# Kernel tuning notes

Hardware: AMD Instinct MI355X
Metric: run time of the kernel (lower is better)

Reference implementation:

```python
import math
import jax, jax.numpy as jnp
import numpy as np

NUM_HEAD = 16

def get_slopes(n):
    def pow2(n):
        start = 2 ** (-2 ** (-(math.log2(n) - 3)))
        return [start * start ** i for i in range(n)]
    if math.log2(n).is_integer():
        return pow2(n)
    c = 2 ** math.floor(math.log2(n))
    return pow2(c) + get_slopes(2 * c)[0::2][: n - c]

def setup_inputs() -> dict:
    key = jax.random.key(0)
    ks = jax.random.split(key, 9)
    B, T, C = 2, 2048, 2048
    x = jax.random.normal(ks[0], (B, T, C), dtype=jnp.float32)
    std = 0.02
    Wq = std * jax.random.normal(ks[1], (C, C), dtype=jnp.float32)
    Wk = std * jax.random.normal(ks[2], (C, C), dtype=jnp.float32)
    Wv = std * jax.random.normal(ks[3], (C, C), dtype=jnp.float32)
    Wo = (0.02 / np.sqrt(2 * 24)) * jax.random.normal(ks[4], (C, C), dtype=jnp.float32)
    bq = jnp.zeros((C,), jnp.float32)
    bk = jnp.zeros((C,), jnp.float32)
    bv = jnp.zeros((C,), jnp.float32)
    bo = jnp.zeros((C,), jnp.float32)
    return {"x": x, "Wq": Wq, "bq": bq, "Wk": Wk, "bk": bk,
            "Wv": Wv, "bv": bv, "Wo": Wo, "bo": bo}

def reference(x, Wq, bq, Wk, bk, Wv, bv, Wo, bo):
    B, T, C = x.shape
    H = NUM_HEAD
    D = C // H
    slopes = jnp.asarray(get_slopes(H), dtype=jnp.float32)  # [H]

    def split_heads(y):  # [B,T,C] -> [B,H,T,D]
        return y.reshape(B, T, H, D).transpose(0, 2, 1, 3)

    q = split_heads(x @ Wq + bq)
    k = split_heads(x @ Wk + bk)
    v = split_heads(x @ Wv + bv)

    attn = jnp.einsum("bhqd,bhkd->bhqk", q, k) / jnp.sqrt(jnp.float32(D))
    # ALiBi: bias[h, j] = slopes[h] * (j - (T-1)), broadcast over queries
    alibi = slopes[:, None, None] * (jnp.arange(T, dtype=jnp.float32) - (T - 1))[None, None, :]
    attn = attn + alibi  # [B,H,T,T] + [H,1,T]

    causal = jnp.tril(jnp.ones((T, T), dtype=bool))[None, None]
    attn = jnp.where(causal, attn, jnp.finfo(jnp.float32).min)
    p = jax.nn.softmax(attn, axis=-1)

    o = jnp.einsum("bhqk,bhkd->bhqd", p, v).transpose(0, 2, 1, 3).reshape(B, T, C)
    return o @ Wo + bo
```

## Files before the change

kernel.cpp:

```cpp
#include <hip/hip_runtime.h>
#include <math.h>


typedef unsigned short u16;
using bf16x8 = __attribute__((ext_vector_type(8))) short;
using f32x4  = __attribute__((ext_vector_type(4))) float;

__device__ __forceinline__ u16 f2bf(float f) {
  union { float f; unsigned u; } c; c.f = f;
  unsigned r = c.u + 0x7fffu + ((c.u >> 16) & 1u);
  return (u16)(r >> 16);
}
__device__ __forceinline__ float bf2f(u16 b) {
  union { unsigned u; float f; } c; c.u = ((unsigned)b) << 16; return c.f;
}
__device__ __forceinline__ unsigned cvtpk(float a, float b) {
  unsigned r;
  asm("v_cvt_pk_bf16_f32 %0, %1, %2" : "=v"(r) : "v"(a), "v"(b));
  return r;
}
__device__ __forceinline__ void g2l16(const void* g, void* l) {
  __builtin_amdgcn_global_load_lds(
      (const __attribute__((address_space(1))) void*)g,
      (__attribute__((address_space(3))) void*)l, 16, 0, 0);
}

__device__ __forceinline__ int band_jmin(int s, float slope2) {
  const int idist = (int)(36.0f / slope2);
  const int cut = 64 * s - idist - 31;
  return (cut > 0) ? (cut >> 5) : 0;
}

__global__ __launch_bounds__(256) void split_f32(const float* __restrict__ in,
                                                 u16* __restrict__ hi, int n4) {
  for (int i = blockIdx.x * 256 + threadIdx.x; i < n4; i += gridDim.x * 256) {
    const float4 v = ((const float4*)in)[i];
    ushort4 h;
    h.x = f2bf(v.x); h.y = f2bf(v.y); h.z = f2bf(v.z); h.w = f2bf(v.w);
    ((ushort4*)hi)[i] = h;
  }
}

__global__ __launch_bounds__(256) void tsplit4_f32(
    const float* __restrict__ W0, const float* __restrict__ W1,
    const float* __restrict__ W2, const float* __restrict__ W3,
    u16* __restrict__ D0, u16* __restrict__ D1,
    u16* __restrict__ D2, u16* __restrict__ D3,
    int N, int K, float sc0) {
  __shared__ float tile[64][68];
  const int z = blockIdx.z;
  const float* W = (z == 0) ? W0 : (z == 1) ? W1 : (z == 2) ? W2 : W3;
  u16* Wth = (z == 0) ? D0 : (z == 1) ? D1 : (z == 2) ? D2 : D3;
  const float sc = (z == 0) ? sc0 : 1.f;
  const int tid = threadIdx.x;
  const int k0 = blockIdx.y * 64, n0 = blockIdx.x * 64;
  const int rr = tid >> 4, cc = (tid & 15) * 4;
#pragma unroll
  for (int u = 0; u < 4; ++u) {
    const float4 v = *(const float4*)&W[(size_t)(k0 + rr + 16 * u) * N + n0 + cc];
    tile[rr + 16 * u][cc + 0] = v.x;
    tile[rr + 16 * u][cc + 1] = v.y;
    tile[rr + 16 * u][cc + 2] = v.z;
    tile[rr + 16 * u][cc + 3] = v.w;
  }
  __syncthreads();
#pragma unroll
  for (int u = 0; u < 4; ++u) {
    const int nn = rr + 16 * u;
    ushort4 h;
    h.x = f2bf(tile[cc + 0][nn] * sc);
    h.y = f2bf(tile[cc + 1][nn] * sc);
    h.z = f2bf(tile[cc + 2][nn] * sc);
    h.w = f2bf(tile[cc + 3][nn] * sc);
    *(ushort4*)&Wth[(size_t)(n0 + nn) * K + k0 + cc] = h;
  }
}

template <int MODE>
__global__ __launch_bounds__(512, 2) void gemm256(
    const u16* __restrict__ Ah, const u16* __restrict__ Bth,
    const float* __restrict__ bias, const float* __restrict__ bias2,
    float bsc, u16* __restrict__ outH, u16* __restrict__ outH2,
    float* __restrict__ outF, int MM, int NN, int KK) {
  __shared__ u16 LA[2][2][8192];
  __shared__ u16 LB[2][2][8192];

  const int tid = threadIdx.x;
  const int wave = tid >> 6, lane = tid & 63;
  const int g = lane >> 4, q15 = lane & 15;
  const int wr = wave >> 2, wc = wave & 3;
  const int m0 = blockIdx.y * 256, n0 = blockIdx.x * 256;
  const int NT = KK >> 6;

  f32x4 acc[8][4];
#pragma unroll
  for (int f = 0; f < 8; ++f)
#pragma unroll
    for (int j = 0; j < 4; ++j) acc[f][j] = (f32x4){0.f, 0.f, 0.f, 0.f};

  auto stageA = [&](int t, int hh) {
#pragma unroll
    for (int l = 0; l < 2; ++l) {
      const int ch = l * 512 + tid;
      const int row = ch >> 3, slot = ch & 7;
      const size_t ga = (size_t)(m0 + hh * 128 + row) * KK + t * 64 +
                        ((slot ^ (row & 7)) * 8);
      g2l16(Ah + ga, (char*)(LA[t & 1][hh]) + ch * 16);
    }
  };
  auto stageB = [&](int t, int hh) {
#pragma unroll
    for (int l = 0; l < 2; ++l) {
      const int ch = l * 512 + tid;
      const int row = ch >> 3, slot = ch & 7;
      const size_t gb = (size_t)(n0 + hh * 128 + row) * KK + t * 64 +
                        ((slot ^ (row & 7)) * 8);
      g2l16(Bth + gb, (char*)(LB[t & 1][hh]) + ch * 16);
    }
  };

  stageA(0, 0); stageA(0, 1); stageB(0, 0); stageB(0, 1);
  asm volatile("s_waitcnt vmcnt(0)" ::: "memory");
  __builtin_amdgcn_sched_barrier(0);
  __builtin_amdgcn_s_barrier();

  for (int t = 0; t < NT; ++t) {
    const int d = t & 1;
    const char* baseA = (const char*)(LA[d][wr]);
    const char* baseB = (const char*)(LB[d][wc >> 1]);
    const int rbBase = (wc & 1) * 64;
    const int sx = q15 & 7;
#pragma unroll
    for (int p = 0; p < 4; ++p) {
      const int mh = p >> 1, nh = p & 1;
      bf16x8 af[4][2], bf[2][2];
#pragma unroll
      for (int f = 0; f < 4; ++f) {
        const int rowh = mh * 64 + f * 16 + q15;
#pragma unroll
        for (int kk = 0; kk < 2; ++kk)
          af[f][kk] = *(const bf16x8*)(baseA + rowh * 128 +
                                       (((kk * 4 + g) ^ sx) * 16));
      }
#pragma unroll
      for (int j = 0; j < 2; ++j) {
        const int rowh = rbBase + nh * 32 + j * 16 + q15;
#pragma unroll
        for (int kk = 0; kk < 2; ++kk)
          bf[j][kk] = *(const bf16x8*)(baseB + rowh * 128 +
                                       (((kk * 4 + g) ^ sx) * 16));
      }
      if (t + 1 < NT) {
        if (p == 0) { stageA(t + 1, 0); stageA(t + 1, 1); }
        else if (p == 1) stageB(t + 1, 0);
        else if (p == 2) stageB(t + 1, 1);
      }
      __builtin_amdgcn_sched_barrier(0);
      __builtin_amdgcn_s_barrier();
      asm volatile("s_waitcnt lgkmcnt(0)" ::: "memory");
      __builtin_amdgcn_sched_barrier(0);
      __builtin_amdgcn_s_setprio(1);
#pragma unroll
      for (int f = 0; f < 4; ++f)
#pragma unroll
        for (int j = 0; j < 2; ++j)
#pragma unroll
          for (int kk = 0; kk < 2; ++kk)
            acc[mh * 4 + f][nh * 2 + j] = __builtin_amdgcn_mfma_f32_16x16x32_bf16(
                af[f][kk], bf[j][kk], acc[mh * 4 + f][nh * 2 + j], 0, 0, 0);
      __builtin_amdgcn_s_setprio(0);
      if (p == 3) {
        asm volatile("s_waitcnt vmcnt(0)" ::: "memory");
      }
      __builtin_amdgcn_sched_barrier(0);
      __builtin_amdgcn_s_barrier();
    }
  }

#pragma unroll
  for (int f = 0; f < 8; ++f)
#pragma unroll
    for (int j = 0; j < 4; ++j)
#pragma unroll
      for (int r = 0; r < 4; ++r) {
        const int row = m0 + wr * 128 + f * 16 + g * 4 + r;
        const int col = n0 + wc * 64 + j * 16 + q15;
        const float v = acc[f][j][r];
        if (MODE == 3) {
          const int sel = col >> 11;
          const int c2 = col & 2047;
          const float vv = v + (sel ? bias2[c2] : bias[c2] * bsc);
          const int bb = row >> 11, tt = row & 2047;
          const int hh = c2 >> 7, dd = c2 & 127;
          (sel ? outH2 : outH)[(((size_t)bb * 16 + hh) * 2048 + tt) * 128 + dd] =
              f2bf(vv);
        }
      }
}

template <int MODE>
__global__ __launch_bounds__(512) void gemm256x128(
    const u16* __restrict__ Ah, const u16* __restrict__ Bth,
    const float* __restrict__ bias, float bsc,
    u16* __restrict__ outH, float* __restrict__ outF,
    int MM, int NN, int KK) {
  __shared__ u16 LA[2][2][8192];
  __shared__ u16 LB[2][8192];

  const int tid = threadIdx.x;
  const int wave = tid >> 6, lane = tid & 63;
  const int g = lane >> 4, q15 = lane & 15;
  const int wr = wave >> 1, wc = wave & 1;
  const int m0 = blockIdx.y * 256, n0 = blockIdx.x * 128;
  const int NT = KK >> 6;

  f32x4 acc[4][4];
#pragma unroll
  for (int f = 0; f < 4; ++f)
#pragma unroll
    for (int j = 0; j < 4; ++j) acc[f][j] = (f32x4){0.f, 0.f, 0.f, 0.f};

  auto stageA = [&](int t, int hh) {
#pragma unroll
    for (int l = 0; l < 2; ++l) {
      const int ch = l * 512 + tid;
      const int row = ch >> 3, slot = ch & 7;
      const size_t ga = (size_t)(m0 + hh * 128 + row) * KK + t * 64 +
                        ((slot ^ (row & 7)) * 8);
      g2l16(Ah + ga, (char*)(LA[t & 1][hh]) + ch * 16);
    }
  };
  auto stageB = [&](int t) {
#pragma unroll
    for (int l = 0; l < 2; ++l) {
      const int ch = l * 512 + tid;
      const int row = ch >> 3, slot = ch & 7;
      const size_t gb = (size_t)(n0 + row) * KK + t * 64 +
                        ((slot ^ (row & 7)) * 8);
      g2l16(Bth + gb, (char*)(LB[t & 1]) + ch * 16);
    }
  };

  stageA(0, 0); stageA(0, 1); stageB(0);
  asm volatile("s_waitcnt vmcnt(0)" ::: "memory");
  __builtin_amdgcn_sched_barrier(0);
  __builtin_amdgcn_s_barrier();

  for (int t = 0; t < NT; ++t) {
    const int d = t & 1;
    const char* baseA = (const char*)(LA[d][wr >> 1]);
    const int raBase = (wr & 1) * 64;
    const char* baseB = (const char*)(LB[d]);
    const int rbBase = wc * 64;
    const int sx = q15 & 7;
#pragma unroll
    for (int p = 0; p < 4; ++p) {
      const int mq = p >> 1, nq = p & 1;
      bf16x8 af[2][2], bf[2][2];
#pragma unroll
      for (int f = 0; f < 2; ++f) {
        const int rowh = raBase + mq * 32 + f * 16 + q15;
#pragma unroll
        for (int kk = 0; kk < 2; ++kk)
          af[f][kk] = *(const bf16x8*)(baseA + rowh * 128 +
                                       (((kk * 4 + g) ^ sx) * 16));
      }
#pragma unroll
      for (int j = 0; j < 2; ++j) {
        const int rowh = rbBase + nq * 32 + j * 16 + q15;
#pragma unroll
        for (int kk = 0; kk < 2; ++kk)
          bf[j][kk] = *(const bf16x8*)(baseB + rowh * 128 +
                                       (((kk * 4 + g) ^ sx) * 16));
      }
      if (t + 1 < NT) {
        if (p == 0) stageA(t + 1, 0);
        else if (p == 1) stageA(t + 1, 1);
        else if (p == 2) stageB(t + 1);
      }
      __builtin_amdgcn_sched_barrier(0);
      __builtin_amdgcn_s_barrier();
      asm volatile("s_waitcnt lgkmcnt(0)" ::: "memory");
      __builtin_amdgcn_sched_barrier(0);
      __builtin_amdgcn_s_setprio(1);
#pragma unroll
      for (int f = 0; f < 2; ++f)
#pragma unroll
        for (int j = 0; j < 2; ++j)
#pragma unroll
          for (int kk = 0; kk < 2; ++kk)
            acc[mq * 2 + f][nq * 2 + j] = __builtin_amdgcn_mfma_f32_16x16x32_bf16(
                af[f][kk], bf[j][kk], acc[mq * 2 + f][nq * 2 + j], 0, 0, 0);
      __builtin_amdgcn_s_setprio(0);
      if (p == 3) {
        asm volatile("s_waitcnt vmcnt(0)" ::: "memory");
      }
      __builtin_amdgcn_sched_barrier(0);
      __builtin_amdgcn_s_barrier();
    }
  }

#pragma unroll
  for (int f = 0; f < 4; ++f)
#pragma unroll
    for (int j = 0; j < 4; ++j)
#pragma unroll
      for (int r = 0; r < 4; ++r) {
        const int row = m0 + wr * 64 + f * 16 + g * 4 + r;
        const int col = n0 + wc * 64 + j * 16 + q15;
        const float v = acc[f][j][r];
        if (MODE == 0) {
          outF[(size_t)row * NN + col] = v + bias[col] * bsc;
        } else {
          outH[(size_t)row * NN + col] = f2bf(v + bias[row] * bsc);
        }
      }
}

__global__ __launch_bounds__(128) void attn_splitk(
    const u16* __restrict__ Qh, const u16* __restrict__ Kh,
    const u16* __restrict__ Vth, u16* __restrict__ Oh,
    float* __restrict__ Obuf, float* __restrict__ mArr,
    float* __restrict__ lArr, int T, int NB, int BH) {
  __shared__ u16 KS[3][4096];

  const int tid = threadIdx.x;
  const int wid = tid >> 6, lane = tid & 63;
  const int g = lane >> 4, q15 = lane & 15;
  const int L = blockIdx.x;

  int bh, u;
  if (BH == 32) {
    const int k = L >> 8;
    const int c = L & 255;
    bh = (c + 5 * k) & 31;
    u = k * 8 + (c >> 5);
  } else {
    bh = L / 48;
    u = L % 48;
  }
  int s, half;
  if (u < 16)      { s = u;      half = 2; }
  else if (u < 32) { s = 47 - u; half = 0; }
  else             { s = 63 - u; half = 1; }

  const int b = bh >> 4, h = bh & 15;
  const float slope2 = exp2f(-0.5f * (float)(h + 1)) * 1.44269504f;
  const int jmin = band_jmin(s, slope2);
  const bool loEmpty = (jmin >= s + 1);

  if (half == 0 && loEmpty) return;

  int lo, hi;
  if (half == 2)      { lo = jmin;                hi = 2 * s + 2; }
  else if (half == 0) { lo = jmin;                hi = s + 1; }
  else                { lo = loEmpty ? jmin : (s + 1); hi = 2 * s + 2; }
  const int ns = hi - lo;
  const bool maskable = (half != 0);
  const bool normStore = (half == 2) || (half == 1 && loEmpty);

  const int qw0 = s * 64 + wid * 32;
  const size_t vrow0 = (size_t)h * 128;
  const size_t vcol0 = (size_t)b * T;
  const size_t kbase = (size_t)bh * T;

  bf16x8 qfr[2][4];
#pragma unroll
  for (int qf2 = 0; qf2 < 2; ++qf2) {
    const size_t rb = ((size_t)bh * T + qw0 + qf2 * 16 + q15) * 128;
#pragma unroll
    for (int ks = 0; ks < 4; ++ks)
      qfr[qf2][ks] = *(const bf16x8*)&Qh[rb + ks * 32 + g * 8];
  }

  f32x4 oacc[2][8];
#pragma unroll
  for (int a = 0; a < 2; ++a)
#pragma unroll
    for (int n = 0; n < 8; ++n) oacc[a][n] = (f32x4){0.f, 0.f, 0.f, 0.f};
  float m_st[2] = {-1e5f, -1e5f};
  float l_part[2] = {0.f, 0.f};

  float sc8[2][4];
#pragma unroll
  for (int jf = 0; jf < 2; ++jf)
#pragma unroll
    for (int r = 0; r < 4; ++r) sc8[jf][r] = slope2 * (float)(jf * 16 + r);

  auto stageK = [&](int jt, int bf) {
    const int j0 = jt * 32;
#pragma unroll
    for (int uu = 0; uu < 4; ++uu) {
      const int c = wid * 4 + uu;
      const int row = c * 4 + g;
      const int off = (q15 * 16) ^ ((row & 7) << 4);
      const size_t gb = (kbase + j0 + row) * 128;
      g2l16((const char*)(Kh + gb) + off, (char*)(KS[bf]) + c * 1024);
    }
  };
  auto loadV = [&](int jt, bf16x8 (&vf)[8]) {
    const int j0 = jt * 32;
#pragma unroll
    for (int nf = 0; nf < 8; ++nf)
      vf[nf] = *(const bf16x8*)
          &Vth[(vrow0 + nf * 16 + q15) * (size_t)NB + vcol0 + j0 + g * 8];
  };

  bf16x8 vfA[8], vfB[8];
  __builtin_amdgcn_sched_barrier(0);
  stageK(hi - 1, 0);
  if (ns > 1) stageK(hi - 2, 1);
  __builtin_amdgcn_sched_barrier(0);
  loadV(hi - 1, vfA);
  asm volatile("s_waitcnt vmcnt(8)" ::: "memory");
  __builtin_amdgcn_sched_barrier(0);

  int cur = 0;

  auto ITER = [&](int it, bf16x8 (&vc)[8], bf16x8 (&vn)[8]) {
    const int jt = hi - 1 - it;
    const int j0 = jt * 32;
    __builtin_amdgcn_s_barrier();
    __builtin_amdgcn_sched_barrier(0);

    const bool haveV1 = (it + 1 < ns);
    const bool haveK2 = (it + 2 < ns);
    if (haveV1) loadV(jt - 1, vn);
    if (haveK2) {
      int nb = cur + 2; if (nb >= 3) nb -= 3;
      stageK(jt - 2, nb);
    }
    __builtin_amdgcn_sched_barrier(0);

    f32x4 sacc[2][2];
#pragma unroll
    for (int jf = 0; jf < 2; ++jf)
#pragma unroll
      for (int qf2 = 0; qf2 < 2; ++qf2) sacc[jf][qf2] = (f32x4){0.f, 0.f, 0.f, 0.f};
#pragma unroll
    for (int ks = 0; ks < 4; ++ks) {
      bf16x8 ka[2];
#pragma unroll
      for (int jf = 0; jf < 2; ++jf) {
        const int row = jf * 16 + q15;
        const int off = (row * 256 + ks * 64 + g * 16) ^ ((row & 7) << 4);
        ka[jf] = *(const bf16x8*)((const char*)(KS[cur]) + off);
      }
#pragma unroll
      for (int jf = 0; jf < 2; ++jf)
#pragma unroll
        for (int qf2 = 0; qf2 < 2; ++qf2)
          sacc[jf][qf2] = __builtin_amdgcn_mfma_f32_16x16x32_bf16(
              ka[jf], qfr[qf2][ks], sacc[jf][qf2], 0, 0, 0);
    }

    float a8[2][4];
    const float jb = (float)(j0 + 4 * g - (T - 1));
#pragma unroll
    for (int jf = 0; jf < 2; ++jf)
#pragma unroll
      for (int r = 0; r < 4; ++r) a8[jf][r] = fmaf(slope2, jb, sc8[jf][r]);

    unsigned Fw[2][4];
#pragma unroll
    for (int qf2 = 0; qf2 < 2; ++qf2) {
      const int qg = qw0 + qf2 * 16 + q15;
      float sv[2][4];
      float mt = -1e30f;
#pragma unroll
      for (int jf = 0; jf < 2; ++jf)
#pragma unroll
        for (int r = 0; r < 4; ++r) {
          float x = sacc[jf][qf2][r] + a8[jf][r];
          if (maskable && it < 2) {
            const int jg = j0 + jf * 16 + 4 * g + r;
            x = (jg > qg) ? -1e30f : x;
          }
          sv[jf][r] = x;
          mt = fmaxf(mt, x);
        }
      if (!__all(mt <= m_st[qf2] + 11.0f)) {
        mt = fmaxf(mt, __shfl_xor(mt, 16));
        mt = fmaxf(mt, __shfl_xor(mt, 32));
        const float mnew = fmaxf(m_st[qf2], mt);
        const float scl = exp2f(m_st[qf2] - mnew);
        l_part[qf2] *= scl;
        m_st[qf2] = mnew;
#pragma unroll
        for (int r = 0; r < 4; ++r) {
          const float sc = __shfl(scl, g * 4 + r);
#pragma unroll
          for (int nf = 0; nf < 8; ++nf) oacc[qf2][nf][r] *= sc;
        }
      }
      float rs = 0.f;
      float p[2][4];
#pragma unroll
      for (int jf = 0; jf < 2; ++jf)
#pragma unroll
        for (int r = 0; r < 4; ++r) {
          p[jf][r] = exp2f(sv[jf][r] - m_st[qf2]);
          rs += p[jf][r];
        }
      l_part[qf2] += rs;
      const unsigned W00 = cvtpk(p[0][0], p[0][1]), W01 = cvtpk(p[0][2], p[0][3]);
      const unsigned W10 = cvtpk(p[1][0], p[1][1]), W11 = cvtpk(p[1][2], p[1][3]);
      const int srcA = q15 + ((g & 1) << 5);
      const int srcB = srcA + 16;
      const unsigned A0 = (unsigned)__shfl((int)W00, srcA);
      const unsigned A1 = (unsigned)__shfl((int)W01, srcA);
      const unsigned B0 = (unsigned)__shfl((int)W00, srcB);
      const unsigned B1 = (unsigned)__shfl((int)W01, srcB);
      const unsigned C0 = (unsigned)__shfl((int)W10, srcA);
      const unsigned C1 = (unsigned)__shfl((int)W11, srcA);
      const unsigned D0 = (unsigned)__shfl((int)W10, srcB);
      const unsigned D1 = (unsigned)__shfl((int)W11, srcB);
      const bool hi2 = g >= 2;
      Fw[qf2][0] = hi2 ? C0 : A0;
      Fw[qf2][1] = hi2 ? C1 : A1;
      Fw[qf2][2] = hi2 ? D0 : B0;
      Fw[qf2][3] = hi2 ? D1 : B1;
    }

    if (haveV1) {
      if (haveK2) { asm volatile("s_waitcnt vmcnt(12)" ::: "memory"); }
      else        { asm volatile("s_waitcnt vmcnt(8)"  ::: "memory"); }
    } else        { asm volatile("s_waitcnt vmcnt(0)"  ::: "memory"); }
    __builtin_amdgcn_sched_barrier(0);

    union { unsigned uu[4]; bf16x8 v; } pa0, pa1;
#pragma unroll
    for (int w = 0; w < 4; ++w) { pa0.uu[w] = Fw[0][w]; pa1.uu[w] = Fw[1][w]; }
#pragma unroll
    for (int nf = 0; nf < 8; ++nf) {
      oacc[0][nf] = __builtin_amdgcn_mfma_f32_16x16x32_bf16(pa0.v, vc[nf], oacc[0][nf], 0, 0, 0);
      oacc[1][nf] = __builtin_amdgcn_mfma_f32_16x16x32_bf16(pa1.v, vc[nf], oacc[1][nf], 0, 0, 0);
    }

    cur = (cur == 2) ? 0 : cur + 1;
  };

  for (int it = 0; it < ns;) {
    ITER(it, vfA, vfB); ++it;
    if (it >= ns) break;
    ITER(it, vfB, vfA); ++it;
  }

  float lrow[2];
#pragma unroll
  for (int qf2 = 0; qf2 < 2; ++qf2) {
    float lr = l_part[qf2];
    lr += __shfl_xor(lr, 16);
    lr += __shfl_xor(lr, 32);
    lrow[qf2] = lr;
  }

  if (normStore) {
#pragma unroll
    for (int qf2 = 0; qf2 < 2; ++qf2) {
      const float inv = 1.0f / lrow[qf2];
#pragma unroll
      for (int r = 0; r < 4; ++r) {
        const float iv = __shfl(inv, g * 4 + r);
        const int qrow = qw0 + qf2 * 16 + g * 4 + r;
        const size_t ob = ((size_t)b * T + qrow) * 2048 + h * 128;
#pragma unroll
        for (int nf = 0; nf < 8; ++nf)
          Oh[ob + nf * 16 + q15] = f2bf(oacc[qf2][nf][r] * iv);
      }
    }
  } else {
    const int sp = s - 16;
    const size_t sbase = ((size_t)(bh * 16 + sp) * 2 + half) * 64;
    if (g == 0) {
#pragma unroll
      for (int qf2 = 0; qf2 < 2; ++qf2) {
        mArr[sbase + wid * 32 + qf2 * 16 + q15] = m_st[qf2];
        lArr[sbase + wid * 32 + qf2 * 16 + q15] = lrow[qf2];
      }
    }
    const size_t obase = sbase * 128;
#pragma unroll
    for (int qf2 = 0; qf2 < 2; ++qf2)
#pragma unroll
      for (int r = 0; r < 4; ++r) {
        const int row = wid * 32 + qf2 * 16 + g * 4 + r;
#pragma unroll
        for (int nf = 0; nf < 8; ++nf)
          Obuf[obase + (size_t)row * 128 + nf * 16 + q15] = oacc[qf2][nf][r];
      }
  }
}

__global__ __launch_bounds__(128) void combine_halves(
    const float* __restrict__ Obuf, const float* __restrict__ mArr,
    const float* __restrict__ lArr, u16* __restrict__ Oh, int T) {
  const int idx = blockIdx.x;
  const int row = idx & 63;
  const int sp = (idx >> 6) & 15;
  const int bh = idx >> 10;
  const int d = threadIdx.x;
  const int s = sp + 16;
  const int b = bh >> 4, h = bh & 15;
  const float slope2 = exp2f(-0.5f * (float)(h + 1)) * 1.44269504f;
  if (band_jmin(s, slope2) >= s + 1) return;
  const size_t sbase = ((size_t)(bh * 16 + sp) * 2) * 64;
  const float m1 = mArr[sbase + row],      l1 = lArr[sbase + row];
  const float m2 = mArr[sbase + 64 + row], l2 = lArr[sbase + 64 + row];
  const float M = fmaxf(m1, m2);
  const float w1 = exp2f(m1 - M), w2 = exp2f(m2 - M);
  const float inv = 1.0f / (l1 * w1 + l2 * w2);
  const size_t ob = sbase * 128;
  const float o1 = Obuf[ob + (size_t)row * 128 + d];
  const float o2 = Obuf[ob + 8192 + (size_t)row * 128 + d];
  const float v = (o1 * w1 + o2 * w2) * inv;
  const int qrow = s * 64 + row;
  Oh[((size_t)b * T + qrow) * 2048 + h * 128 + d] = f2bf(v);
}

#define TM 128
#define BKG 8

template <int QKV>
__global__ __launch_bounds__(256) void gemm_f32(
    const float* __restrict__ A, const float* __restrict__ W,
    const float* __restrict__ bias, float* __restrict__ out,
    int M, int N, int K, int T) {
  __shared__ float As[BKG][TM];
  __shared__ float Bs[BKG][TM];
  const int tid = threadIdx.x;
  const int tx = tid & 15, ty = tid >> 4;
  const int m0 = blockIdx.y * TM, n0 = blockIdx.x * TM;
  float acc[8][8];
#pragma unroll
  for (int i = 0; i < 8; ++i)
#pragma unroll
    for (int j = 0; j < 8; ++j) acc[i][j] = 0.f;
  const int arow = tid >> 1, acol = (tid & 1) * 4;
  const int brow = tid >> 5, bcol = (tid & 31) * 4;
  for (int k0 = 0; k0 < K; k0 += BKG) {
    const float4 av = *(const float4*)&A[(size_t)(m0 + arow) * K + k0 + acol];
    const float4 bv = *(const float4*)&W[(size_t)(k0 + brow) * N + n0 + bcol];
    __syncthreads();
    As[acol + 0][arow] = av.x; As[acol + 1][arow] = av.y;
    As[acol + 2][arow] = av.z; As[acol + 3][arow] = av.w;
    *(float4*)&Bs[brow][bcol] = bv;
    __syncthreads();
#pragma unroll
    for (int kk = 0; kk < BKG; ++kk) {
      const float4 a0 = *(const float4*)&As[kk][ty * 4];
      const float4 a1 = *(const float4*)&As[kk][64 + ty * 4];
      const float4 b0 = *(const float4*)&Bs[kk][tx * 4];
      const float4 b1 = *(const float4*)&Bs[kk][64 + tx * 4];
      const float af[8] = {a0.x, a0.y, a0.z, a0.w, a1.x, a1.y, a1.z, a1.w};
      const float bf[8] = {b0.x, b0.y, b0.z, b0.w, b1.x, b1.y, b1.z, b1.w};
#pragma unroll
      for (int i = 0; i < 8; ++i)
#pragma unroll
        for (int j = 0; j < 8; ++j) acc[i][j] += af[i] * bf[j];
    }
  }
#pragma unroll
  for (int a = 0; a < 2; ++a)
#pragma unroll
    for (int i = 0; i < 4; ++i) {
      const int row = m0 + a * 64 + ty * 4 + i;
      const int bb = row / T, t = row % T;
#pragma unroll
      for (int bj = 0; bj < 2; ++bj) {
        const int col = n0 + bj * 64 + tx * 4;
        float4 r;
        r.x = acc[a * 4 + i][bj * 4 + 0] + bias[col + 0];
        r.y = acc[a * 4 + i][bj * 4 + 1] + bias[col + 1];
        r.z = acc[a * 4 + i][bj * 4 + 2] + bias[col + 2];
        r.w = acc[a * 4 + i][bj * 4 + 3] + bias[col + 3];
        if (QKV) {
          const int hh = col >> 7, dd = col & 127;
          *(float4*)&out[(((size_t)bb * 16 + hh) * T + t) * 128 + dd] = r;
        } else {
          *(float4*)&out[(size_t)row * N + col] = r;
        }
      }
    }
}

#define QT 32
#define KT 32
#define DP 132

__global__ __launch_bounds__(256) void flash_f32(
    const float* __restrict__ Q, const float* __restrict__ K,
    const float* __restrict__ V, float* __restrict__ O, int T) {
  __shared__ float Qs[QT][DP];
  __shared__ float Ks[KT][DP];
  __shared__ float Vs[KT][DP];
  __shared__ float Ps[QT][KT + 1];
  const int tid = threadIdx.x;
  const int jh = tid & 15, ih = tid >> 4;
  const int bh = blockIdx.y;
  const int h = bh & 15;
  const int q0 = blockIdx.x * QT;
  const float slope = exp2f(-0.5f * (float)(h + 1));
  const float rsD = 0.08838834764831845f;
  {
    const float* Qg = Q + ((size_t)bh * T + q0) * 128;
    const int r = tid >> 3, p = tid & 7;
#pragma unroll
    for (int u = 0; u < 4; ++u)
      *(float4*)&Qs[r][(p + 8 * u) * 4] = *(const float4*)&Qg[r * 128 + (p + 8 * u) * 4];
  }
  float m_st[2] = {-1e30f, -1e30f};
  float l_st[2] = {0.f, 0.f};
  float accv[2][8] = {};
  const int ktiles = blockIdx.x + 1;
  for (int kt = 0; kt < ktiles; ++kt) {
    const int j0 = kt * KT;
    const float* Kg = K + ((size_t)bh * T + j0) * 128;
    const float* Vg = V + ((size_t)bh * T + j0) * 128;
    __syncthreads();
    {
      const int r = tid >> 3, p = tid & 7;
#pragma unroll
      for (int u = 0; u < 4; ++u) {
        *(float4*)&Ks[r][(p + 8 * u) * 4] = *(const float4*)&Kg[r * 128 + (p + 8 * u) * 4];
        *(float4*)&Vs[r][(p + 8 * u) * 4] = *(const float4*)&Vg[r * 128 + (p + 8 * u) * 4];
      }
    }
    __syncthreads();
    float s00 = 0.f, s01 = 0.f, s10 = 0.f, s11 = 0.f;
#pragma unroll 8
    for (int d4 = 0; d4 < 32; ++d4) {
      const float4 qa = *(const float4*)&Qs[2 * ih + 0][4 * d4];
      const float4 qb = *(const float4*)&Qs[2 * ih + 1][4 * d4];
      const float4 ka = *(const float4*)&Ks[2 * jh + 0][4 * d4];
      const float4 kb = *(const float4*)&Ks[2 * jh + 1][4 * d4];
      s00 += qa.x * ka.x + qa.y * ka.y + qa.z * ka.z + qa.w * ka.w;
      s01 += qa.x * kb.x + qa.y * kb.y + qa.z * kb.z + qa.w * kb.w;
      s10 += qb.x * ka.x + qb.y * ka.y + qb.z * ka.z + qb.w * ka.w;
      s11 += qb.x * kb.x + qb.y * kb.y + qb.z * kb.z + qb.w * kb.w;
    }
    float sc[2][2] = {{s00, s01}, {s10, s11}};
    float mt[2];
#pragma unroll
    for (int r = 0; r < 2; ++r) {
      const int qg = q0 + 2 * ih + r;
#pragma unroll
      for (int c = 0; c < 2; ++c) {
        const int jg = j0 + 2 * jh + c;
        const float svv = sc[r][c] * rsD + slope * (float)(jg - (T - 1));
        sc[r][c] = (jg > qg) ? -1e30f : svv;
      }
      mt[r] = fmaxf(sc[r][0], sc[r][1]);
    }
#pragma unroll
    for (int m = 1; m < 16; m <<= 1) {
      mt[0] = fmaxf(mt[0], __shfl_xor(mt[0], m));
      mt[1] = fmaxf(mt[1], __shfl_xor(mt[1], m));
    }
#pragma unroll
    for (int r = 0; r < 2; ++r) {
      const float mnew = fmaxf(m_st[r], mt[r]);
      const float scl = (m_st[r] > -1e29f) ? expf(m_st[r] - mnew) : 0.f;
      const float p0 = expf(sc[r][0] - mnew);
      const float p1 = expf(sc[r][1] - mnew);
      float rs = p0 + p1;
#pragma unroll
      for (int m = 1; m < 16; m <<= 1) rs += __shfl_xor(rs, m);
      l_st[r] = l_st[r] * scl + rs;
      m_st[r] = mnew;
#pragma unroll
      for (int d = 0; d < 8; ++d) accv[r][d] *= scl;
      Ps[2 * ih + r][2 * jh + 0] = p0;
      Ps[2 * ih + r][2 * jh + 1] = p1;
    }
    __syncthreads();
#pragma unroll 4
    for (int j = 0; j < KT; ++j) {
      const float p0 = Ps[2 * ih + 0][j];
      const float p1 = Ps[2 * ih + 1][j];
      const float4 v0 = *(const float4*)&Vs[j][8 * jh];
      const float4 v1 = *(const float4*)&Vs[j][8 * jh + 4];
      accv[0][0] += p0 * v0.x; accv[0][1] += p0 * v0.y;
      accv[0][2] += p0 * v0.z; accv[0][3] += p0 * v0.w;
      accv[0][4] += p0 * v1.x; accv[0][5] += p0 * v1.y;
      accv[0][6] += p0 * v1.z; accv[0][7] += p0 * v1.w;
      accv[1][0] += p1 * v0.x; accv[1][1] += p1 * v0.y;
      accv[1][2] += p1 * v0.z; accv[1][3] += p1 * v0.w;
      accv[1][4] += p1 * v1.x; accv[1][5] += p1 * v1.y;
      accv[1][6] += p1 * v1.z; accv[1][7] += p1 * v1.w;
    }
  }
  const int b = bh >> 4;
#pragma unroll
  for (int r = 0; r < 2; ++r) {
    const int qg = q0 + 2 * ih + r;
    const float inv = 1.0f / l_st[r];
    float4 o0, o1;
    o0.x = accv[r][0] * inv; o0.y = accv[r][1] * inv;
    o0.z = accv[r][2] * inv; o0.w = accv[r][3] * inv;
    o1.x = accv[r][4] * inv; o1.y = accv[r][5] * inv;
    o1.z = accv[r][6] * inv; o1.w = accv[r][7] * inv;
    float* dst = O + ((size_t)b * T + qg) * 2048 + h * 128 + 8 * jh;
    *(float4*)&dst[0] = o0;
    *(float4*)&dst[4] = o1;
  }
}

extern "C" void kernel_launch(void* const* d_in, const int* in_sizes, int n_in,
                              void* d_out, int out_size, void* d_ws,
                              size_t ws_size, hipStream_t stream) {
  const float* x  = (const float*)d_in[0];
  const float* Wq = (const float*)d_in[1];
  const float* bq = (const float*)d_in[2];
  const float* Wk = (const float*)d_in[3];
  const float* bk = (const float*)d_in[4];
  const float* Wv = (const float*)d_in[5];
  const float* bv = (const float*)d_in[6];
  const float* Wo = (const float*)d_in[7];
  const float* bo = (const float*)d_in[8];
  float* out = (float*)d_out;

  const int C = 2048, T = 2048, H = 16;
  const int M = in_sizes[0] / C;
  const int B = M / T;
  const int BH = B * H;
  const size_t MC = (size_t)M * C, CC = (size_t)C * C;
  const size_t splitO = (size_t)BH * 16 * 2 * 8192;
  const size_t splitML = (size_t)BH * 16 * 2 * 64;
  const size_t need = (5 * MC + 4 * CC) * sizeof(u16) +
                      (splitO + 2 * splitML) * sizeof(float);

  const float QSC = 0.08838834764831845f * 1.44269504088896f;

  if (ws_size >= need && (M % 256) == 0) {
    u16* p = (u16*)d_ws;
    u16* xh   = p; p += MC;
    u16* wqth = p; p += CC;
    u16* wkth = p; p += CC;
    u16* wvth = p; p += CC;
    u16* woth = p; p += CC;
    u16* qh   = p; p += MC;
    u16* kh   = p; p += MC;
    u16* vth  = p; p += MC;
    u16* oh   = p; p += MC;
    float* Obuf = (float*)p;
    float* mArr = Obuf + splitO;
    float* lArr = mArr + splitML;

    split_f32<<<1024, 256, 0, stream>>>(x, xh, (int)(MC / 4));
    dim3 tg(C / 64, C / 64, 4);
    tsplit4_f32<<<tg, 256, 0, stream>>>(Wq, Wk, Wv, Wo, wqth, wkth, wvth,
                                        woth, C, C, QSC);

    dim3 gqk(2 * C / 256, M / 256);
    gemm256<3><<<gqk, 512, 0, stream>>>(xh, wqth, bq, bk, QSC, qh, kh,
                                        nullptr, M, 2 * C, C);
    dim3 gv(M / 128, C / 256);
    gemm256x128<2><<<gv, 512, 0, stream>>>(wvth, xh, bv, 1.f, vth, nullptr,
                                           C, M, C);

    attn_splitk<<<48 * BH, 128, 0, stream>>>(qh, kh, vth, oh, Obuf, mArr,
                                             lArr, T, M, BH);
    combine_halves<<<BH * 16 * 64, 128, 0, stream>>>(Obuf, mArr, lArr, oh, T);

    dim3 gq(C / 128, M / 256);
    gemm256x128<0><<<gq, 512, 0, stream>>>(oh, woth, bo, 1.f, nullptr, out,
                                           M, C, C);
  } else {
    float* Qw = (float*)d_ws;
    float* Kw = Qw + MC;
    float* Vw = Kw + MC;
    float* Ow = Vw + MC;
    dim3 ggrid(C / TM, M / TM);
    gemm_f32<1><<<ggrid, 256, 0, stream>>>(x, Wq, bq, Qw, M, C, C, T);
    gemm_f32<1><<<ggrid, 256, 0, stream>>>(x, Wk, bk, Kw, M, C, C, T);
    gemm_f32<1><<<ggrid, 256, 0, stream>>>(x, Wv, bv, Vw, M, C, C, T);
    dim3 fgrid(T / QT, B * H);
    flash_f32<<<fgrid, 256, 0, stream>>>(Qw, Kw, Vw, Ow, T);
    gemm_f32<0><<<ggrid, 256, 0, stream>>>(Ow, Wo, bo, out, M, C, C, T);
  }
}
```

Before: 315.6 us.

## Use 4-stage LDS ring with K=32 tiles and prefetch depth 3 in GEMMs

Both bf16 GEMM kernels move from a double-buffered K=64 tile to a four-slot ring of K=32 tiles. Global-to-LDS loads are issued three tiles ahead, and partial vmcnt waits replace a full drain every iteration. The LDS swizzle and fragment-load layout change to match the 64-byte rows. This is meant to hide more global memory latency, at the cost of twice as many iterations and barriers, plus more intricate wait-count bookkeeping.

```diff
diff --git a/kernel.cpp b/kernel.cpp
--- a/kernel.cpp
+++ b/kernel.cpp
@@ -82,15 +82,16 @@
     const float* __restrict__ bias, const float* __restrict__ bias2,
     float bsc, u16* __restrict__ outH, u16* __restrict__ outH2,
     float* __restrict__ outF, int MM, int NN, int KK) {
-  __shared__ u16 LA[2][2][8192];
-  __shared__ u16 LB[2][2][8192];
+  __shared__ u16 LA[4][8192];
+  __shared__ u16 LB[4][8192];
 
   const int tid = threadIdx.x;
   const int wave = tid >> 6, lane = tid & 63;
   const int g = lane >> 4, q15 = lane & 15;
   const int wr = wave >> 2, wc = wave & 3;
   const int m0 = blockIdx.y * 256, n0 = blockIdx.x * 256;
-  const int NT = KK >> 6;
+  const int NT = KK >> 5;
+  const int sxg = ((g ^ ((q15 >> 1) & 3)) << 4);
 
   f32x4 acc[8][4];
 #pragma unroll
@@ -98,83 +99,93 @@
 #pragma unroll
     for (int j = 0; j < 4; ++j) acc[f][j] = (f32x4){0.f, 0.f, 0.f, 0.f};
 
-  auto stageA = [&](int t, int hh) {
+  auto stageA = [&](int t) {
+    const int rb = t & 3;
 #pragma unroll
     for (int l = 0; l < 2; ++l) {
       const int ch = l * 512 + tid;
-      const int row = ch >> 3, slot = ch & 7;
-      const size_t ga = (size_t)(m0 + hh * 128 + row) * KK + t * 64 +
-                        ((slot ^ (row & 7)) * 8);
-      g2l16(Ah + ga, (char*)(LA[t & 1][hh]) + ch * 16);
+      const int row = ch >> 2, slot = ch & 3;
+      const size_t ga = (size_t)(m0 + row) * KK + t * 32 +
+                        ((slot ^ ((row >> 1) & 3)) * 8);
+      g2l16(Ah + ga, (char*)(LA[rb]) + ch * 16);
     }
   };
-  auto stageB = [&](int t, int hh) {
+  auto stageB = [&](int t) {
+    const int rb = t & 3;
 #pragma unroll
     for (int l = 0; l < 2; ++l) {
       const int ch = l * 512 + tid;
-      const int row = ch >> 3, slot = ch & 7;
-      const size_t gb = (size_t)(n0 + hh * 128 + row) * KK + t * 64 +
-                        ((slot ^ (row & 7)) * 8);
-      g2l16(Bth + gb, (char*)(LB[t & 1][hh]) + ch * 16);
+      const int row = ch >> 2, slot = ch & 3;
+      const size_t gb = (size_t)(n0 + row) * KK + t * 32 +
+                        ((slot ^ ((row >> 1) & 3)) * 8);
+      g2l16(Bth + gb, (char*)(LB[rb]) + ch * 16);
     }
   };
 
-  stageA(0, 0); stageA(0, 1); stageB(0, 0); stageB(0, 1);
-  asm volatile("s_waitcnt vmcnt(0)" ::: "memory");
+  stageA(0); stageB(0);
+  __builtin_amdgcn_sched_barrier(0);
+  if (NT > 1) { stageA(1); stageB(1); }
+  __builtin_amdgcn_sched_barrier(0);
+  if (NT > 2) { stageA(2); stageB(2); }
+  __builtin_amdgcn_sched_barrier(0);
+  if (NT > 2)      { asm volatile("s_waitcnt vmcnt(8)" ::: "memory"); }
+  else if (NT > 1) { asm volatile("s_waitcnt vmcnt(4)" ::: "memory"); }
+  else             { asm volatile("s_waitcnt vmcnt(0)" ::: "memory"); }
   __builtin_amdgcn_sched_barrier(0);
   __builtin_amdgcn_s_barrier();
 
   for (int t = 0; t < NT; ++t) {
-    const int d = t & 1;
-    const char* baseA = (const char*)(LA[d][wr]);
-    const char* baseB = (const char*)(LB[d][wc >> 1]);
-    const int rbBase = (wc & 1) * 64;
-    const int sx = q15 & 7;
-#pragma unroll
-    for (int p = 0; p < 4; ++p) {
-      const int mh = p >> 1, nh = p & 1;
-      bf16x8 af[4][2], bf[2][2];
-#pragma unroll
-      for (int f = 0; f < 4; ++f) {
-        const int rowh = mh * 64 + f * 16 + q15;
-#pragma unroll
-        for (int kk = 0; kk < 2; ++kk)
-          af[f][kk] = *(const bf16x8*)(baseA + rowh * 128 +
-                                       (((kk * 4 + g) ^ sx) * 16));
-      }
-#pragma unroll
-      for (int j = 0; j < 2; ++j) {
-        const int rowh = rbBase + nh * 32 + j * 16 + q15;
-#pragma unroll
-        for (int kk = 0; kk < 2; ++kk)
-          bf[j][kk] = *(const bf16x8*)(baseB + rowh * 128 +
-                                       (((kk * 4 + g) ^ sx) * 16));
-      }
-      if (t + 1 < NT) {
-        if (p == 0) { stageA(t + 1, 0); stageA(t + 1, 1); }
-        else if (p == 1) stageB(t + 1, 0);
-        else if (p == 2) stageB(t + 1, 1);
-      }
-      __builtin_amdgcn_sched_barrier(0);
-      __builtin_amdgcn_s_barrier();
-      asm volatile("s_waitcnt lgkmcnt(0)" ::: "memory");
-      __builtin_amdgcn_sched_barrier(0);
-      __builtin_amdgcn_s_setprio(1);
-#pragma unroll
-      for (int f = 0; f < 4; ++f)
-#pragma unroll
-        for (int j = 0; j < 2; ++j)
-#pragma unroll
-          for (int kk = 0; kk < 2; ++kk)
-            acc[mh * 4 + f][nh * 2 + j] = __builtin_amdgcn_mfma_f32_16x16x32_bf16(
-                af[f][kk], bf[j][kk], acc[mh * 4 + f][nh * 2 + j], 0, 0, 0);
-      __builtin_amdgcn_s_setprio(0);
-      if (p == 3) {
-        asm volatile("s_waitcnt vmcnt(0)" ::: "memory");
-      }
-      __builtin_amdgcn_sched_barrier(0);
-      __builtin_amdgcn_s_barrier();
-    }
+    const int rb = t & 3;
+    const char* baseA = (const char*)(LA[rb]);
+    const char* baseB = (const char*)(LB[rb]);
+
+    bf16x8 bf[4], af[4];
+#pragma unroll
+    for (int j = 0; j < 4; ++j)
+      bf[j] = *(const bf16x8*)(baseB + (wc * 64 + j * 16 + q15) * 64 + sxg);
+#pragma unroll
+    for (int f = 0; f < 4; ++f)
+      af[f] = *(const bf16x8*)(baseA + (wr * 128 + f * 16 + q15) * 64 + sxg);
+    if (t + 3 < NT) stageA(t + 3);
+    __builtin_amdgcn_sched_barrier(0);
+    __builtin_amdgcn_s_barrier();
+    asm volatile("s_waitcnt lgkmcnt(0)" ::: "memory");
+    __builtin_amdgcn_sched_barrier(0);
+    __builtin_amdgcn_s_setprio(1);
+#pragma unroll
+    for (int f = 0; f < 4; ++f)
+#pragma unroll
+      for (int j = 0; j < 4; ++j)
+        acc[f][j] = __builtin_amdgcn_mfma_f32_16x16x32_bf16(
+            af[f], bf[j], acc[f][j], 0, 0, 0);
+    __builtin_amdgcn_s_setprio(0);
+    __builtin_amdgcn_sched_barrier(0);
+    __builtin_amdgcn_s_barrier();
+
+    bf16x8 ag[4];
+#pragma unroll
+    for (int f = 0; f < 4; ++f)
+      ag[f] = *(const bf16x8*)(baseA + (wr * 128 + 64 + f * 16 + q15) * 64 + sxg);
+    if (t + 3 < NT) stageB(t + 3);
+    __builtin_amdgcn_sched_barrier(0);
+    __builtin_amdgcn_s_barrier();
+    asm volatile("s_waitcnt lgkmcnt(0)" ::: "memory");
+    __builtin_amdgcn_sched_barrier(0);
+    __builtin_amdgcn_s_setprio(1);
+#pragma unroll
+    for (int f = 0; f < 4; ++f)
+#pragma unroll
+      for (int j = 0; j < 4; ++j)
+        acc[4 + f][j] = __builtin_amdgcn_mfma_f32_16x16x32_bf16(
+            ag[f], bf[j], acc[4 + f][j], 0, 0, 0);
+    __builtin_amdgcn_s_setprio(0);
+    if (t + 1 < NT) {
+      if (t + 4 <= NT)      { asm volatile("s_waitcnt vmcnt(8)" ::: "memory"); }
+      else if (t + 3 <= NT) { asm volatile("s_waitcnt vmcnt(4)" ::: "memory"); }
+      else                  { asm volatile("s_waitcnt vmcnt(0)" ::: "memory"); }
+    }
+    __builtin_amdgcn_sched_barrier(0);
+    __builtin_amdgcn_s_barrier();
   }
 
 #pragma unroll
@@ -204,15 +215,16 @@
     const float* __restrict__ bias, float bsc,
     u16* __restrict__ outH, float* __restrict__ outF,
     int MM, int NN, int KK) {
-  __shared__ u16 LA[2][2][8192];
-  __shared__ u16 LB[2][8192];
+  __shared__ u16 LA[4][8192];
+  __shared__ u16 LB[4][4096];
 
   const int tid = threadIdx.x;
   const int wave = tid >> 6, lane = tid & 63;
   const int g = lane >> 4, q15 = lane & 15;
   const int wr = wave >> 1, wc = wave & 1;
   const int m0 = blockIdx.y * 256, n0 = blockIdx.x * 128;
-  const int NT = KK >> 6;
+  const int NT = KK >> 5;
+  const int sxg = ((g ^ ((q15 >> 1) & 3)) << 4);
 
   f32x4 acc[4][4];
 #pragma unroll
@@ -220,84 +232,70 @@
 #pragma unroll
     for (int j = 0; j < 4; ++j) acc[f][j] = (f32x4){0.f, 0.f, 0.f, 0.f};
 
-  auto stageA = [&](int t, int hh) {
+  auto stageA = [&](int t) {
+    const int rb = t & 3;
 #pragma unroll
     for (int l = 0; l < 2; ++l) {
       const int ch = l * 512 + tid;
-      const int row = ch >> 3, slot = ch & 7;
-      const size_t ga = (size_t)(m0 + hh * 128 + row) * KK + t * 64 +
-                        ((slot ^ (row & 7)) * 8);
-      g2l16(Ah + ga, (char*)(LA[t & 1][hh]) + ch * 16);
+      const int row = ch >> 2, slot = ch & 3;
+      const size_t ga = (size_t)(m0 + row) * KK + t * 32 +
+                        ((slot ^ ((row >> 1) & 3)) * 8);
+      g2l16(Ah + ga, (char*)(LA[rb]) + ch * 16);
     }
   };
   auto stageB = [&](int t) {
-#pragma unroll
-    for (int l = 0; l < 2; ++l) {
-      const int ch = l * 512 + tid;
-      const int row = ch >> 3, slot = ch & 7;
-      const size_t gb = (size_t)(n0 + row) * KK + t * 64 +
-                        ((slot ^ (row & 7)) * 8);
-      g2l16(Bth + gb, (char*)(LB[t & 1]) + ch * 16);
-    }
+    const int rb = t & 3;
+    const int ch = tid;
+    const int row = ch >> 2, slot = ch & 3;
+    const size_t gb = (size_t)(n0 + row) * KK + t * 32 +
+                      ((slot ^ ((row >> 1) & 3)) * 8);
+    g2l16(Bth + gb, (char*)(LB[rb]) + ch * 16);
   };
 
-  stageA(0, 0); stageA(0, 1); stageB(0);
-  asm volatile("s_waitcnt vmcnt(0)" ::: "memory");
+  stageA(0); stageB(0);
+  __builtin_amdgcn_sched_barrier(0);
+  if (NT > 1) { stageA(1); stageB(1); }
+  __builtin_amdgcn_sched_barrier(0);
+  if (NT > 2) { stageA(2); stageB(2); }
+  __builtin_amdgcn_sched_barrier(0);
+  if (NT > 2)      { asm volatile("s_waitcnt vmcnt(6)" ::: "memory"); }
+  else if (NT > 1) { asm volatile("s_waitcnt vmcnt(3)" ::: "memory"); }
+  else             { asm volatile("s_waitcnt vmcnt(0)" ::: "memory"); }
   __builtin_amdgcn_sched_barrier(0);
   __builtin_amdgcn_s_barrier();
 
   for (int t = 0; t < NT; ++t) {
-    const int d = t & 1;
-    const char* baseA = (const char*)(LA[d][wr >> 1]);
-    const int raBase = (wr & 1) * 64;
-    const char* baseB = (const char*)(LB[d]);
-    const int rbBase = wc * 64;
-    const int sx = q15 & 7;
-#pragma unroll
-    for (int p = 0; p < 4; ++p) {
-      const int mq = p >> 1, nq = p & 1;
-      bf16x8 af[2][2], bf[2][2];
-#pragma unroll
-      for (int f = 0; f < 2; ++f) {
-        const int rowh = raBase + mq * 32 + f * 16 + q15;
-#pragma unroll
-        for (int kk = 0; kk < 2; ++kk)
-          af[f][kk] = *(const bf16x8*)(baseA + rowh * 128 +
-                                       (((kk * 4 + g) ^ sx) * 16));
-      }
-#pragma unroll
-      for (int j = 0; j < 2; ++j) {
-        const int rowh = rbBase + nq * 32 + j * 16 + q15;
-#pragma unroll
-        for (int kk = 0; kk < 2; ++kk)
-          bf[j][kk] = *(const bf16x8*)(baseB + rowh * 128 +
-                                       (((kk * 4 + g) ^ sx) * 16));
-      }
-      if (t + 1 < NT) {
-        if (p == 0) stageA(t + 1, 0);
-        else if (p == 1) stageA(t + 1, 1);
-        else if (p == 2) stageB(t + 1);
-      }
-      __builtin_amdgcn_sched_barrier(0);
-      __builtin_amdgcn_s_barrier();
-      asm volatile("s_waitcnt lgkmcnt(0)" ::: "memory");
-      __builtin_amdgcn_sched_barrier(0);
-      __builtin_amdgcn_s_setprio(1);
-#pragma unroll
-      for (int f = 0; f < 2; ++f)
-#pragma unroll
-        for (int j = 0; j < 2; ++j)
-#pragma unroll
-          for (int kk = 0; kk < 2; ++kk)
-            acc[mq * 2 + f][nq * 2 + j] = __builtin_amdgcn_mfma_f32_16x16x32_bf16(
-                af[f][kk], bf[j][kk], acc[mq * 2 + f][nq * 2 + j], 0, 0, 0);
-      __builtin_amdgcn_s_setprio(0);
-      if (p == 3) {
-        asm volatile("s_waitcnt vmcnt(0)" ::: "memory");
-      }
-      __builtin_amdgcn_sched_barrier(0);
-      __builtin_amdgcn_s_barrier();
-    }
+    const int rb = t & 3;
+    const char* baseA = (const char*)(LA[rb]);
+    const char* baseB = (const char*)(LB[rb]);
+
+    bf16x8 af[4], bf[4];
+#pragma unroll
+    for (int f = 0; f < 4; ++f)
+      af[f] = *(const bf16x8*)(baseA + (wr * 64 + f * 16 + q15) * 64 + sxg);
+#pragma unroll
+    for (int j = 0; j < 4; ++j)
+      bf[j] = *(const bf16x8*)(baseB + (wc * 64 + j * 16 + q15) * 64 + sxg);
+    if (t + 3 < NT) { stageA(t + 3); stageB(t + 3); }
+    __builtin_amdgcn_sched_barrier(0);
+    __builtin_amdgcn_s_barrier();
+    asm volatile("s_waitcnt lgkmcnt(0)" ::: "memory");
+    __builtin_amdgcn_sched_barrier(0);
+    __builtin_amdgcn_s_setprio(1);
+#pragma unroll
+    for (int f = 0; f < 4; ++f)
+#pragma unroll
+      for (int j = 0; j < 4; ++j)
+        acc[f][j] = __builtin_amdgcn_mfma_f32_16x16x32_bf16(
+            af[f], bf[j], acc[f][j], 0, 0, 0);
+    __builtin_amdgcn_s_setprio(0);
+    if (t + 1 < NT) {
+      if (t + 4 <= NT)      { asm volatile("s_waitcnt vmcnt(6)" ::: "memory"); }
+      else if (t + 3 <= NT) { asm volatile("s_waitcnt vmcnt(3)" ::: "memory"); }
+      else                  { asm volatile("s_waitcnt vmcnt(0)" ::: "memory"); }
+    }
+    __builtin_amdgcn_sched_barrier(0);
+    __builtin_amdgcn_s_barrier();
   }
 
 #pragma unroll
```

Result: faster. 298.6 us (-5.4%).
